# Kernel optimization log

Hardware: AMD Instinct MI355X
Metric: run time of the kernel (lower is better)

## Reference

```python
import jax, jax.numpy as jnp
import numpy as np

N, E, IN, OUT, R, B = 20000, 640000, 128, 128, 65, 65
BN_EPS = 1e-5


def setup_inputs() -> dict:
    key = jax.random.key(0)
    ks = jax.random.split(key, 8)
    node_feats = jax.random.normal(ks[0], (N, IN), dtype=jnp.float32)
    src = jax.random.randint(ks[1], (E,), 0, N, dtype=jnp.int32)
    dst = jax.random.randint(ks[2], (E,), 0, N, dtype=jnp.int32)
    etype = jax.random.randint(ks[3], (E,), 0, R, dtype=jnp.int32)
    norm = jax.random.uniform(ks[4], (E, 1), dtype=jnp.float32)
    basis = jax.random.normal(ks[5], (B, IN, OUT), dtype=jnp.float32) * 0.05
    comp = jax.random.normal(ks[6], (R, B), dtype=jnp.float32) * 0.1
    h_bias = jnp.zeros((OUT,), dtype=jnp.float32)
    W_res = jax.random.normal(ks[7], (IN, OUT), dtype=jnp.float32) * 0.05
    b_res = jnp.zeros((OUT,), dtype=jnp.float32)
    gamma = jnp.ones((OUT,), dtype=jnp.float32)
    beta = jnp.zeros((OUT,), dtype=jnp.float32)
    return dict(node_feats=node_feats, src=src, dst=dst, etype=etype, norm=norm,
                basis=basis, comp=comp, h_bias=h_bias, W_res=W_res, b_res=b_res,
                gamma=gamma, beta=beta)


def reference(node_feats, src, dst, etype, norm, basis, comp, h_bias, W_res, b_res, gamma, beta):
    n, in_f = node_feats.shape
    r = comp.shape[0]
    # Basis decomposition: W_r = sum_b comp[r,b] * basis[b]  -> (R, in, out)
    W = jnp.einsum('rb,bio->rio', comp, basis)
    # Per-edge message x[src] * norm (norm is scalar per edge so it commutes
    # with the relation matmul). Aggregate per (dst, relation) first, then do
    # one dense relation-batched GEMM (mathematically identical to DGL's
    # per-edge transform + scatter-add, since everything is linear).
    msg = node_feats[src] * norm                       # (E, in)
    seg = dst.astype(jnp.int32) * r + etype            # combined (dst, rel) key
    S = jax.ops.segment_sum(msg, seg, num_segments=n * r).reshape(n, r, in_f)
    h = jnp.einsum('nri,rio->no', S, W) + h_bias       # (N, out)
    h = jax.nn.relu(h)                                 # conv activation (dropout p=0)
    # Residual branch: relu(Linear(x))
    h = h + jax.nn.relu(node_feats @ W_res + b_res)
    # BatchNorm1d (training mode: batch stats, biased variance)
    mean = jnp.mean(h, axis=0)
    var = jnp.var(h, axis=0)
    h = (h - mean) * jax.lax.rsqrt(var + BN_EPS) * gamma + beta
    return h
```

## Files before the change

### kernel.cpp

```cpp
#include <hip/hip_runtime.h>
#include <hip/hip_bf16.h>


#define N_NODES 20000
#define E_EDGES 640000
#define R_REL   65
#define TM      64
#define NB_RESID 313
#define MAX_TILES 10240
#define SCAT_CH 2560

typedef __attribute__((ext_vector_type(8))) short bf16x8;
typedef __attribute__((ext_vector_type(4))) float f32x4;
typedef __attribute__((ext_vector_type(4))) unsigned int u32x4;
typedef __attribute__((ext_vector_type(2))) unsigned int u32x2;

__device__ __forceinline__ unsigned short f2bf(float x) {
    union { float f; unsigned int u; } c; c.f = x;
    unsigned int b = c.u + 0x7fffu + ((c.u >> 16) & 1u);
    return (unsigned short)(b >> 16);
}
__device__ __forceinline__ float bf2f_lo(unsigned int u) {
    union { unsigned int u; float f; } c; c.u = u << 16; return c.f;
}
__device__ __forceinline__ float bf2f_hi(unsigned int u) {
    union { unsigned int u; float f; } c; c.u = u & 0xffff0000u; return c.f;
}
__device__ __forceinline__ void async16(const void* g, void* l) {
    __builtin_amdgcn_global_load_lds(
        (const __attribute__((address_space(1))) unsigned int*)g,
        (__attribute__((address_space(3))) unsigned int*)l, 16, 0, 0);
}
__device__ __forceinline__ int unperm(int p) {
    return (p & 64) + ((p & 3) << 4) + ((p >> 2) & 15);
}

__global__ void k_prep1(const float* __restrict__ comp, const float* __restrict__ basis,
                        float* __restrict__ W32, const int* __restrict__ et,
                        const int* __restrict__ dstA, int* __restrict__ ghist,
                        int* __restrict__ gh2, const float* __restrict__ node_feats,
                        unsigned short* __restrict__ node_bf) {
    __shared__ float lc[16 * 65];
    __shared__ int lh[R_REL];
    int b = blockIdx.x, t = threadIdx.x;
    if (b < 320) {
        int r0 = (b >> 6) * 16;
        int col = (b & 63) * 256 + t;
        for (int j = t; j < 16 * 65; j += 256) {
            int rr = r0 + j / 65;
            lc[j] = (rr < R_REL) ? comp[rr * 65 + (j % 65)] : 0.f;
        }
        __syncthreads();
        float acc[16];
#pragma unroll
        for (int j = 0; j < 16; ++j) acc[j] = 0.f;
        for (int k = 0; k < 65; ++k) {
            float v = basis[k * 16384 + col];
#pragma unroll
            for (int j = 0; j < 16; ++j) acc[j] += lc[j * 65 + k] * v;
        }
#pragma unroll
        for (int j = 0; j < 16; ++j) {
            int rr = r0 + j;
            if (rr < R_REL) W32[rr * 16384 + col] = acc[j];
        }
    } else if (b < 832) {
        if (t < R_REL) lh[t] = 0;
        __syncthreads();
        for (int i = (b - 320) * 256 + t; i < E_EDGES; i += 512 * 256) {
            atomicAdd(&lh[et[i]], 1);
            atomicAdd(&gh2[dstA[i]], 1);
        }
        __syncthreads();
        if (t < R_REL) atomicAdd(&ghist[t], lh[t]);
    } else {
        int i = (b - 832) * 256 + t;
        if (i < N_NODES * 32) {
            float4 v = reinterpret_cast<const float4*>(node_feats)[i];
            __hip_bfloat162 b0 = __float22bfloat162_rn(make_float2(v.x, v.y));
            __hip_bfloat162 b1 = __float22bfloat162_rn(make_float2(v.z, v.w));
            u32x2 pk;
            pk.x = *reinterpret_cast<unsigned int*>(&b0);
            pk.y = *reinterpret_cast<unsigned int*>(&b1);
            reinterpret_cast<u32x2*>(node_bf)[i] = pk;
        }
    }
}

__global__ void k_prep2(const float* __restrict__ W32, unsigned short* __restrict__ Wt,
                        const float* __restrict__ Wresf, unsigned short* __restrict__ Wrest,
                        const int* __restrict__ gh2, int* __restrict__ bsum) {
    int b = blockIdx.x, t = threadIdx.x;
    if (b < 264) {
        __shared__ float tile[64][65];
        const float* s; unsigned short* d; int sub;
        if (b < R_REL * 4) { s = W32 + (size_t)(b >> 2) * 16384; d = Wt + (size_t)(b >> 2) * 16384; sub = b & 3; }
        else { s = Wresf; d = Wrest; sub = b - R_REL * 4; }
        int ot = (sub >> 1) & 1, itl = sub & 1;
        int tx = t & 63, ty = t >> 6;
        for (int it = 0; it < 16; ++it) {
            int i = ty + it * 4;
            tile[i][tx] = s[(itl * 64 + i) * 128 + ot * 64 + tx];
        }
        __syncthreads();
        for (int it = 0; it < 16; ++it) {
            int o = ty + it * 4;
            d[(ot * 64 + o) * 128 + itl * 64 + tx] = f2bf(tile[tx][o]);
        }
    } else {
        __shared__ int red[256];
        int i = (b - 264) * 256 + t;
        red[t] = (i < N_NODES) ? gh2[i] : 0;
        __syncthreads();
        for (int off = 128; off > 0; off >>= 1) {
            if (t < off) red[t] += red[t + off];
            __syncthreads();
        }
        if (t == 0) bsum[b - 264] = red[0];
    }
}

__global__ void k_prep3(const int* __restrict__ gh2, const int* __restrict__ bsum,
                        int* __restrict__ cnt2, int* __restrict__ seg,
                        const int* __restrict__ ghist, int* __restrict__ cnt,
                        int* __restrict__ ntiles_p, int* __restrict__ tile_rel,
                        int* __restrict__ tile_start, int* __restrict__ tile_len) {
    int b = blockIdx.x, t = threadIdx.x;
    if (b < 80) {
        __shared__ int red[256], spref;
        if (t < 64) {
            int v = (t < b) ? bsum[t] : 0;
            if (t < 16 && 64 + t < b) v += bsum[64 + t];
#pragma unroll
            for (int off = 1; off < 64; off <<= 1) v += __shfl_xor(v, off);
            if (t == 0) spref = v;
        }
        int i = b * 256 + t;
        int v = (i < N_NODES) ? gh2[i] : 0;
        red[t] = v;
        __syncthreads();
        for (int off = 1; off < 256; off <<= 1) {
            int x = (t >= off) ? red[t - off] : 0;
            __syncthreads();
            red[t] += x;
            __syncthreads();
        }
        int excl = red[t] - v + spref;
        if (i < N_NODES) {
            cnt2[i] = excl;
            seg[i] = excl;
            if (i == N_NODES - 1) seg[N_NODES] = excl + v;
        }
    } else {
        __shared__ int base[R_REL + 1], tbase[R_REL + 1];
        int lane = t & 63;
        if (t < 64) {
            int v = (lane < 64) ? ghist[lane] : 0;
            int x = v;
#pragma unroll
            for (int off = 1; off < 64; off <<= 1) {
                int y = __shfl_up(x, off);
                if (lane >= off) x += y;
            }
            base[lane] = x - v;
            if (lane == 63) {
                base[64] = x;
                base[65] = x + ghist[64];
            }
        }
        __syncthreads();
        if (t == 0) {
            int tb = 0;
            for (int r = 0; r < R_REL; ++r) {
                tbase[r] = tb;
                tb += (base[r + 1] - base[r] + TM - 1) / TM;
            }
            *ntiles_p = tb;
        }
        __syncthreads();
        if (t < R_REL) {
            cnt[t] = base[t];
            int s = base[t], e = base[t + 1], j = tbase[t];
            while (s < e) {
                int len = min(TM, e - s);
                tile_rel[j] = t; tile_start[j] = s; tile_len[j] = len;
                ++j; s += len;
            }
        }
    }
}

__global__ void k_scatter2(const int* __restrict__ et, const int* __restrict__ srcA,
                           const int* __restrict__ dstA, const float* __restrict__ norm,
                           int* __restrict__ cnt, int* __restrict__ cnt2,
                           int* __restrict__ srcp, float* __restrict__ normp,
                           int* __restrict__ inv2) {
    __shared__ int lh[R_REL], lbase[R_REL];
    int c0 = blockIdx.x * SCAT_CH;
    int cend = min(c0 + SCAT_CH, E_EDGES);
    if (threadIdx.x < R_REL) lh[threadIdx.x] = 0;
    __syncthreads();
    for (int i = c0 + threadIdx.x; i < cend; i += 256) atomicAdd(&lh[et[i]], 1);
    __syncthreads();
    if (threadIdx.x < R_REL && lh[threadIdx.x] > 0)
        lbase[threadIdx.x] = atomicAdd(&cnt[threadIdx.x], lh[threadIdx.x]);
    __syncthreads();
    if (threadIdx.x < R_REL) lh[threadIdx.x] = 0;
    __syncthreads();
    for (int i = c0 + threadIdx.x; i < cend; i += 256) {
        int r = et[i];
        int p = lbase[r] + atomicAdd(&lh[r], 1);
        srcp[p] = srcA[i];
        normp[p] = norm[i];
        inv2[p] = atomicAdd(&cnt2[dstA[i]], 1);
    }
}

__global__ __launch_bounds__(256, 3) void k_conv_gemm(
    const int* __restrict__ tile_rel, const int* __restrict__ tile_start,
    const int* __restrict__ tile_len, const int* __restrict__ ntiles_p,
    const int* __restrict__ srcp, const float* __restrict__ normp,
    const unsigned short* __restrict__ node_bf,
    const unsigned short* __restrict__ Wt, const unsigned short* __restrict__ Wrest,
    const float* __restrict__ b_res, const int* __restrict__ inv2,
    unsigned short* __restrict__ t_out, float* __restrict__ resid) {
    __shared__ unsigned short Alds[64 * 128];
    __shared__ unsigned short Blds[128 * 128];
    __shared__ float snorm[64];
    __shared__ int sp2[64];
    int t = threadIdx.x;
    int w = t >> 6, lane = t & 63;
    int wr = (w >> 1) * 32, wc = (w & 1) * 64;
    int lrow = lane & 15, quad = lane >> 4;

    if (blockIdx.x < NB_RESID) {
        int row0 = blockIdx.x * 64;
        int nrows = min(64, N_NODES - row0);
#pragma unroll
        for (int it = 0; it < 8; ++it) {
            int j = t + 256 * it;
            int o = j >> 4, c = j & 15, cs = c ^ (o & 15);
            async16(Wrest + o * 128 + cs * 8, &Blds[o * 128 + c * 8]);
        }
#pragma unroll
        for (int it = 0; it < 4; ++it) {
            int j = t + 256 * it;
            int p = j >> 4, c = j & 15, cs = c ^ (p & 15);
            if (p < nrows)
                async16(node_bf + (size_t)(row0 + p) * 128 + cs * 8,
                        &Alds[p * 128 + c * 8]);
        }
        __syncthreads();
        f32x4 acc[2][4];
#pragma unroll
        for (int i = 0; i < 2; ++i)
#pragma unroll
            for (int j = 0; j < 4; ++j) acc[i][j] = (f32x4){0.f, 0.f, 0.f, 0.f};
#pragma unroll
        for (int ks = 0; ks < 4; ++ks) {
            int cs = (ks * 4 + quad) ^ lrow;
            bf16x8 af[2], bfr[4];
#pragma unroll
            for (int i = 0; i < 2; ++i)
                af[i] = *reinterpret_cast<const bf16x8*>(&Alds[(wr + i * 16 + lrow) * 128 + cs * 8]);
#pragma unroll
            for (int j = 0; j < 4; ++j)
                bfr[j] = *reinterpret_cast<const bf16x8*>(&Blds[(wc + j * 16 + lrow) * 128 + cs * 8]);
#pragma unroll
            for (int i = 0; i < 2; ++i)
#pragma unroll
                for (int j = 0; j < 4; ++j)
                    acc[i][j] = __builtin_amdgcn_mfma_f32_16x16x32_bf16(af[i], bfr[j], acc[i][j], 0, 0, 0);
        }
        float br0 = b_res[wc + lrow];
        float br1 = b_res[wc + 16 + lrow];
        float br2 = b_res[wc + 32 + lrow];
        float br3 = b_res[wc + 48 + lrow];
#pragma unroll
        for (int i = 0; i < 2; ++i) {
#pragma unroll
            for (int reg = 0; reg < 4; ++reg) {
                int grow = row0 + wr + i * 16 + quad * 4 + reg;
                if (grow < N_NODES) {
                    float4 v;
                    v.x = fmaxf(acc[i][0][reg] + br0, 0.f);
                    v.y = fmaxf(acc[i][1][reg] + br1, 0.f);
                    v.z = fmaxf(acc[i][2][reg] + br2, 0.f);
                    v.w = fmaxf(acc[i][3][reg] + br3, 0.f);
                    *reinterpret_cast<float4*>(resid + (size_t)grow * 128 + wc + lrow * 4) = v;
                }
            }
        }
        return;
    }

    int tid = blockIdx.x - NB_RESID;
    if (tid >= *ntiles_p) return;
    int r = tile_rel[tid], start = tile_start[tid], len = tile_len[tid];
    const unsigned short* Wr = Wt + (size_t)r * 16384;
#pragma unroll
    for (int it = 0; it < 8; ++it) {
        int j = t + 256 * it;
        int o = j >> 4, c = j & 15, cs = c ^ (o & 15);
        async16(Wr + o * 128 + cs * 8, &Blds[o * 128 + c * 8]);
    }
#pragma unroll
    for (int it = 0; it < 4; ++it) {
        int j = t + 256 * it;
        int p = j >> 4, c = j & 15, cs = c ^ (p & 15);
        if (p < len)
            async16(node_bf + (size_t)srcp[start + p] * 128 + cs * 8,
                    &Alds[p * 128 + c * 8]);
    }
    if (t < TM && t < len) {
        snorm[t] = normp[start + t];
        sp2[t] = inv2[start + t];
    }
    __syncthreads();

    f32x4 acc[2][4];
#pragma unroll
    for (int i = 0; i < 2; ++i)
#pragma unroll
        for (int j = 0; j < 4; ++j) acc[i][j] = (f32x4){0.f, 0.f, 0.f, 0.f};
#pragma unroll
    for (int ks = 0; ks < 4; ++ks) {
        int cs = (ks * 4 + quad) ^ lrow;
        bf16x8 af[2], bfr[4];
#pragma unroll
        for (int i = 0; i < 2; ++i)
            af[i] = *reinterpret_cast<const bf16x8*>(&Alds[(wr + i * 16 + lrow) * 128 + cs * 8]);
#pragma unroll
        for (int j = 0; j < 4; ++j)
            bfr[j] = *reinterpret_cast<const bf16x8*>(&Blds[(wc + j * 16 + lrow) * 128 + cs * 8]);
#pragma unroll
        for (int i = 0; i < 2; ++i)
#pragma unroll
            for (int j = 0; j < 4; ++j)
                acc[i][j] = __builtin_amdgcn_mfma_f32_16x16x32_bf16(af[i], bfr[j], acc[i][j], 0, 0, 0);
    }

#pragma unroll
    for (int i = 0; i < 2; ++i) {
        int m0 = wr + i * 16 + quad * 4;
#pragma unroll
        for (int reg = 0; reg < 4; ++reg) {
            int m = m0 + reg;
            if (m < len) {
                float nm = snorm[m];
                int p2 = sp2[m];
                float2 lo2 = make_float2(acc[i][0][reg] * nm, acc[i][1][reg] * nm);
                float2 hi2 = make_float2(acc[i][2][reg] * nm, acc[i][3][reg] * nm);
                __hip_bfloat162 blo = __float22bfloat162_rn(lo2);
                __hip_bfloat162 bhi = __float22bfloat162_rn(hi2);
                u32x2 st;
                st.x = *reinterpret_cast<unsigned int*>(&blo);
                st.y = *reinterpret_cast<unsigned int*>(&bhi);
                __builtin_nontemporal_store(st,
                    reinterpret_cast<u32x2*>(t_out + (size_t)p2 * 128 + wc + lrow * 4));
            }
        }
    }
}

__global__ __launch_bounds__(256) void k_reduce_fused(
    const unsigned short* __restrict__ t, const int* __restrict__ seg,
    const float* __restrict__ resid, const float* __restrict__ h_bias,
    float* __restrict__ h, float* __restrict__ colsum, float* __restrict__ colsumsq) {
    __shared__ float cs1[128], cs2[128], sbias[128];
    if (threadIdx.x < 128) {
        cs1[threadIdx.x] = 0.f; cs2[threadIdx.x] = 0.f;
        sbias[threadIdx.x] = h_bias[unperm(threadIdx.x)];
    }
    __syncthreads();
    int w = threadIdx.x >> 6, lane = threadIdx.x & 63;
    int g = lane >> 4, c = lane & 15;
    for (int k = 0; k < 4; ++k) {
        int d = blockIdx.x * 16 + k * 4 + w;
        int a = seg[d], b = seg[d + 1];
        float s[8];
#pragma unroll
        for (int kk = 0; kk < 8; ++kk) s[kk] = 0.f;
        int q = a + g;
        for (; q + 12 < b; q += 16) {
            u32x4 v0 = __builtin_nontemporal_load(reinterpret_cast<const u32x4*>(t + (size_t)q * 128 + c * 8));
            u32x4 v1 = __builtin_nontemporal_load(reinterpret_cast<const u32x4*>(t + (size_t)(q + 4) * 128 + c * 8));
            u32x4 v2 = __builtin_nontemporal_load(reinterpret_cast<const u32x4*>(t + (size_t)(q + 8) * 128 + c * 8));
            u32x4 v3 = __builtin_nontemporal_load(reinterpret_cast<const u32x4*>(t + (size_t)(q + 12) * 128 + c * 8));
#pragma unroll
            for (int kk = 0; kk < 4; ++kk) {
                s[2 * kk]     += bf2f_lo(v0[kk]) + bf2f_lo(v1[kk]) + bf2f_lo(v2[kk]) + bf2f_lo(v3[kk]);
                s[2 * kk + 1] += bf2f_hi(v0[kk]) + bf2f_hi(v1[kk]) + bf2f_hi(v2[kk]) + bf2f_hi(v3[kk]);
            }
        }
        for (; q < b; q += 4) {
            u32x4 v = __builtin_nontemporal_load(reinterpret_cast<const u32x4*>(t + (size_t)q * 128 + c * 8));
#pragma unroll
            for (int kk = 0; kk < 4; ++kk) {
                s[2 * kk]     += bf2f_lo(v[kk]);
                s[2 * kk + 1] += bf2f_hi(v[kk]);
            }
        }
#pragma unroll
        for (int kk = 0; kk < 8; ++kk) {
            s[kk] += __shfl_xor(s[kk], 16);
            s[kk] += __shfl_xor(s[kk], 32);
        }
        if (g == 0) {
            const float* rp = resid + (size_t)d * 128 + c * 8;
            float4 r0 = *reinterpret_cast<const float4*>(rp);
            float4 r1 = *reinterpret_cast<const float4*>(rp + 4);
            float rr[8] = {r0.x, r0.y, r0.z, r0.w, r1.x, r1.y, r1.z, r1.w};
            float v[8];
#pragma unroll
            for (int kk = 0; kk < 8; ++kk)
                v[kk] = fmaxf(s[kk] + sbias[c * 8 + kk], 0.f) + rr[kk];
            float* hp = h + (size_t)d * 128 + c * 8;
            *reinterpret_cast<float4*>(hp)     = make_float4(v[0], v[1], v[2], v[3]);
            *reinterpret_cast<float4*>(hp + 4) = make_float4(v[4], v[5], v[6], v[7]);
#pragma unroll
            for (int kk = 0; kk < 8; ++kk) {
                atomicAdd(&cs1[c * 8 + kk], v[kk]);
                atomicAdd(&cs2[c * 8 + kk], v[kk] * v[kk]);
            }
        }
    }
    __syncthreads();
    if (threadIdx.x < 128) {
        atomicAdd(&colsum[threadIdx.x], cs1[threadIdx.x]);
        atomicAdd(&colsumsq[threadIdx.x], cs2[threadIdx.x]);
    }
}

__global__ void k_bn(float* __restrict__ h, const float* __restrict__ colsum,
                     const float* __restrict__ colsumsq, const float* __restrict__ gamma,
                     const float* __restrict__ beta) {
    __shared__ float sc[128], sh[128], tile[8][128];
    int t = threadIdx.x;
    if (t < 128) {
        int n = unperm(t);
        float m = colsum[t] * (1.f / N_NODES);
        float var = colsumsq[t] * (1.f / N_NODES) - m * m;
        float s = gamma[n] * rsqrtf(var + 1e-5f);
        sc[t] = s;
        sh[t] = beta[n] - m * s;
    }
    __syncthreads();
    int r = t >> 5;
    int p0 = (t & 31) * 4;
    int n0 = (p0 & 64) + ((p0 >> 2) & 15);
    for (int row0 = blockIdx.x * 8; row0 < N_NODES; row0 += gridDim.x * 8) {
        int row = row0 + r;
        float4 v = make_float4(0.f, 0.f, 0.f, 0.f);
        if (row < N_NODES) v = *reinterpret_cast<float4*>(h + (size_t)row * 128 + p0);
        v.x = v.x * sc[p0] + sh[p0];
        v.y = v.y * sc[p0 + 1] + sh[p0 + 1];
        v.z = v.z * sc[p0 + 2] + sh[p0 + 2];
        v.w = v.w * sc[p0 + 3] + sh[p0 + 3];
        tile[r][n0]      = v.x;
        tile[r][n0 + 16] = v.y;
        tile[r][n0 + 32] = v.z;
        tile[r][n0 + 48] = v.w;
        __syncthreads();
        if (row < N_NODES)
            *reinterpret_cast<float4*>(h + (size_t)row * 128 + p0) =
                *reinterpret_cast<float4*>(&tile[r][p0]);
        __syncthreads();
    }
}

extern "C" void kernel_launch(void* const* d_in, const int* in_sizes, int n_in,
                              void* d_out, int out_size, void* d_ws, size_t ws_size,
                              hipStream_t stream) {
    (void)in_sizes; (void)n_in; (void)out_size; (void)ws_size;
    const float* node_feats = (const float*)d_in[0];
    const int* src    = (const int*)d_in[1];
    const int* dst    = (const int*)d_in[2];
    const int* etype  = (const int*)d_in[3];
    const float* norm = (const float*)d_in[4];
    const float* basis = (const float*)d_in[5];
    const float* comp  = (const float*)d_in[6];
    const float* h_bias = (const float*)d_in[7];
    const float* W_res  = (const float*)d_in[8];
    const float* b_res  = (const float*)d_in[9];
    const float* gamma  = (const float*)d_in[10];
    const float* beta   = (const float*)d_in[11];

    char* ws = (char*)d_ws;
    int* ghist      = (int*)(ws + 0);
    int* cnt        = (int*)(ws + 1024);
    int* ntiles_p   = (int*)(ws + 2048);
    float* colsum   = (float*)(ws + 2560);
    float* colsumsq = (float*)(ws + 3072);
    int* bsum       = (int*)(ws + 3584);
    int* gh2        = (int*)(ws + 8192);
    int* tile_rel   = (int*)(ws + 88192);
    int* tile_start = (int*)(ws + 129152);
    int* tile_len   = (int*)(ws + 170112);
    unsigned short* Wt      = (unsigned short*)(ws + 211072);
    unsigned short* Wrest   = (unsigned short*)(ws + 2340992);
    unsigned short* node_bf = (unsigned short*)(ws + 2373760);
    int* srcp       = (int*)(ws + 7493760);
    float* normp    = (float*)(ws + 10053760);
    int* inv2       = (int*)(ws + 12613760);
    float* resid    = (float*)(ws + 15173760);
    int* seg        = (int*)(ws + 25413760);
    int* cnt2       = (int*)(ws + 25493776);
    const long T_BASE = 25573776L;
    float* W32      = (float*)(ws + T_BASE);
    unsigned short* t_buf = (unsigned short*)(ws + T_BASE);
    float* hacc = (float*)d_out;

    hipMemsetAsync(ws, 0, 88192, stream);
    k_prep1<<<3332, 256, 0, stream>>>(comp, basis, W32, etype, dst, ghist, gh2,
                                      node_feats, node_bf);
    k_prep2<<<344, 256, 0, stream>>>(W32, Wt, W_res, Wrest, gh2, bsum);
    k_prep3<<<81, 256, 0, stream>>>(gh2, bsum, cnt2, seg, ghist, cnt, ntiles_p,
                                    tile_rel, tile_start, tile_len);
    k_scatter2<<<(E_EDGES + SCAT_CH - 1) / SCAT_CH, 256, 0, stream>>>(
        etype, src, dst, norm, cnt, cnt2, srcp, normp, inv2);
    k_conv_gemm<<<NB_RESID + MAX_TILES, 256, 0, stream>>>(
        tile_rel, tile_start, tile_len, ntiles_p, srcp, normp, node_bf,
        Wt, Wrest, b_res, inv2, t_buf, resid);
    k_reduce_fused<<<N_NODES / 16, 256, 0, stream>>>(t_buf, seg, resid, h_bias,
                                                     hacc, colsum, colsumsq);
    k_bn<<<2500, 256, 0, stream>>>(hacc, colsum, colsumsq, gamma, beta);
}
```

Before: 352.9 us.

## Split conv GEMM tiles into column halves, merge prep kernels, deepen reduce unroll

The conv GEMM now gives each block half of the 128 output columns, which halves the B tile in LDS and the accumulator registers and raises launch bounds to 4 waves per SIMD. The grid doubles, so A gathers and edge metadata are loaded twice per tile. The two prep kernels merge into one, with each scan block recomputing its prefix directly from gh2 instead of using a separate block-sum pass. The reduce loop is unrolled to 8 loads in flight per iteration.

Result: slower. 387.8 us (+9.9%).

```diff
diff --git a/kernel.cpp b/kernel.cpp
--- a/kernel.cpp
+++ b/kernel.cpp
@@ -6,8 +6,8 @@
 #define E_EDGES 640000
 #define R_REL   65
 #define TM      64
-#define NB_RESID 313
-#define MAX_TILES 10240
+#define NB_RESID 626
+#define NB_EDGE  20608
 #define SCAT_CH 2560
 
 typedef __attribute__((ext_vector_type(8))) short bf16x8;
@@ -87,54 +87,27 @@
     }
 }
 
-__global__ void k_prep2(const float* __restrict__ W32, unsigned short* __restrict__ Wt,
-                        const float* __restrict__ Wresf, unsigned short* __restrict__ Wrest,
-                        const int* __restrict__ gh2, int* __restrict__ bsum) {
+__global__ void k_prep3(const int* __restrict__ gh2, int* __restrict__ cnt2,
+                        int* __restrict__ seg, const int* __restrict__ ghist,
+                        int* __restrict__ cnt, int* __restrict__ ntiles_p,
+                        int* __restrict__ tile_rel, int* __restrict__ tile_start,
+                        int* __restrict__ tile_len, const float* __restrict__ W32,
+                        unsigned short* __restrict__ Wt, const float* __restrict__ Wresf,
+                        unsigned short* __restrict__ Wrest) {
     int b = blockIdx.x, t = threadIdx.x;
-    if (b < 264) {
-        __shared__ float tile[64][65];
-        const float* s; unsigned short* d; int sub;
-        if (b < R_REL * 4) { s = W32 + (size_t)(b >> 2) * 16384; d = Wt + (size_t)(b >> 2) * 16384; sub = b & 3; }
-        else { s = Wresf; d = Wrest; sub = b - R_REL * 4; }
-        int ot = (sub >> 1) & 1, itl = sub & 1;
-        int tx = t & 63, ty = t >> 6;
-        for (int it = 0; it < 16; ++it) {
-            int i = ty + it * 4;
-            tile[i][tx] = s[(itl * 64 + i) * 128 + ot * 64 + tx];
-        }
-        __syncthreads();
-        for (int it = 0; it < 16; ++it) {
-            int o = ty + it * 4;
-            d[(ot * 64 + o) * 128 + itl * 64 + tx] = f2bf(tile[tx][o]);
-        }
-    } else {
+    if (b < 80) {
         __shared__ int red[256];
-        int i = (b - 264) * 256 + t;
-        red[t] = (i < N_NODES) ? gh2[i] : 0;
+        __shared__ int pref;
+        int acc = 0;
+        for (int i = t; i < b * 256; i += 256) acc += gh2[i];
+        red[t] = acc;
         __syncthreads();
         for (int off = 128; off > 0; off >>= 1) {
             if (t < off) red[t] += red[t + off];
             __syncthreads();
         }
-        if (t == 0) bsum[b - 264] = red[0];
-    }
-}
-
-__global__ void k_prep3(const int* __restrict__ gh2, const int* __restrict__ bsum,
-                        int* __restrict__ cnt2, int* __restrict__ seg,
-                        const int* __restrict__ ghist, int* __restrict__ cnt,
-                        int* __restrict__ ntiles_p, int* __restrict__ tile_rel,
-                        int* __restrict__ tile_start, int* __restrict__ tile_len) {
-    int b = blockIdx.x, t = threadIdx.x;
-    if (b < 80) {
-        __shared__ int red[256], spref;
-        if (t < 64) {
-            int v = (t < b) ? bsum[t] : 0;
-            if (t < 16 && 64 + t < b) v += bsum[64 + t];
-#pragma unroll
-            for (int off = 1; off < 64; off <<= 1) v += __shfl_xor(v, off);
-            if (t == 0) spref = v;
-        }
+        if (t == 0) pref = red[0];
+        __syncthreads();
         int i = b * 256 + t;
         int v = (i < N_NODES) ? gh2[i] : 0;
         red[t] = v;
@@ -145,17 +118,17 @@
             red[t] += x;
             __syncthreads();
         }
-        int excl = red[t] - v + spref;
+        int excl = red[t] - v + pref;
         if (i < N_NODES) {
             cnt2[i] = excl;
             seg[i] = excl;
             if (i == N_NODES - 1) seg[N_NODES] = excl + v;
         }
-    } else {
+    } else if (b == 80) {
         __shared__ int base[R_REL + 1], tbase[R_REL + 1];
         int lane = t & 63;
         if (t < 64) {
-            int v = (lane < 64) ? ghist[lane] : 0;
+            int v = ghist[lane];
             int x = v;
 #pragma unroll
             for (int off = 1; off < 64; off <<= 1) {
@@ -186,6 +159,23 @@
                 tile_rel[j] = t; tile_start[j] = s; tile_len[j] = len;
                 ++j; s += len;
             }
+        }
+    } else {
+        __shared__ float tile[64][65];
+        int bb = b - 81;
+        const float* s; unsigned short* d; int sub;
+        if (bb < R_REL * 4) { s = W32 + (size_t)(bb >> 2) * 16384; d = Wt + (size_t)(bb >> 2) * 16384; sub = bb & 3; }
+        else { s = Wresf; d = Wrest; sub = bb - R_REL * 4; }
+        int ot = (sub >> 1) & 1, itl = sub & 1;
+        int tx = t & 63, ty = t >> 6;
+        for (int it = 0; it < 16; ++it) {
+            int i = ty + it * 4;
+            tile[i][tx] = s[(itl * 64 + i) * 128 + ot * 64 + tx];
+        }
+        __syncthreads();
+        for (int it = 0; it < 16; ++it) {
+            int o = ty + it * 4;
+            d[(ot * 64 + o) * 128 + itl * 64 + tx] = f2bf(tile[tx][o]);
         }
     }
 }
@@ -216,7 +206,7 @@
     }
 }
 
-__global__ __launch_bounds__(256, 3) void k_conv_gemm(
+__global__ __launch_bounds__(256, 4) void k_conv_gemm(
     const int* __restrict__ tile_rel, const int* __restrict__ tile_start,
     const int* __restrict__ tile_len, const int* __restrict__ ntiles_p,
     const int* __restrict__ srcp, const float* __restrict__ normp,
@@ -225,22 +215,22 @@
     const float* __restrict__ b_res, const int* __restrict__ inv2,
     unsigned short* __restrict__ t_out, float* __restrict__ resid) {
     __shared__ unsigned short Alds[64 * 128];
-    __shared__ unsigned short Blds[128 * 128];
+    __shared__ unsigned short Blds[64 * 128];
     __shared__ float snorm[64];
     __shared__ int sp2[64];
     int t = threadIdx.x;
     int w = t >> 6, lane = t & 63;
-    int wr = (w >> 1) * 32, wc = (w & 1) * 64;
     int lrow = lane & 15, quad = lane >> 4;
 
     if (blockIdx.x < NB_RESID) {
-        int row0 = blockIdx.x * 64;
+        int rt = blockIdx.x >> 1, half = blockIdx.x & 1;
+        int row0 = rt * 64, wc = half * 64;
         int nrows = min(64, N_NODES - row0);
 #pragma unroll
-        for (int it = 0; it < 8; ++it) {
+        for (int it = 0; it < 4; ++it) {
             int j = t + 256 * it;
             int o = j >> 4, c = j & 15, cs = c ^ (o & 15);
-            async16(Wrest + o * 128 + cs * 8, &Blds[o * 128 + c * 8]);
+            async16(Wrest + (size_t)(wc + o) * 128 + cs * 8, &Blds[o * 128 + c * 8]);
         }
 #pragma unroll
         for (int it = 0; it < 4; ++it) {
@@ -251,55 +241,46 @@
                         &Alds[p * 128 + c * 8]);
         }
         __syncthreads();
-        f32x4 acc[2][4];
-#pragma unroll
-        for (int i = 0; i < 2; ++i)
-#pragma unroll
-            for (int j = 0; j < 4; ++j) acc[i][j] = (f32x4){0.f, 0.f, 0.f, 0.f};
+        f32x4 acc[4];
+#pragma unroll
+        for (int j = 0; j < 4; ++j) acc[j] = (f32x4){0.f, 0.f, 0.f, 0.f};
 #pragma unroll
         for (int ks = 0; ks < 4; ++ks) {
             int cs = (ks * 4 + quad) ^ lrow;
-            bf16x8 af[2], bfr[4];
-#pragma unroll
-            for (int i = 0; i < 2; ++i)
-                af[i] = *reinterpret_cast<const bf16x8*>(&Alds[(wr + i * 16 + lrow) * 128 + cs * 8]);
-#pragma unroll
-            for (int j = 0; j < 4; ++j)
-                bfr[j] = *reinterpret_cast<const bf16x8*>(&Blds[(wc + j * 16 + lrow) * 128 + cs * 8]);
-#pragma unroll
-            for (int i = 0; i < 2; ++i)
-#pragma unroll
-                for (int j = 0; j < 4; ++j)
-                    acc[i][j] = __builtin_amdgcn_mfma_f32_16x16x32_bf16(af[i], bfr[j], acc[i][j], 0, 0, 0);
+            bf16x8 af = *reinterpret_cast<const bf16x8*>(&Alds[(w * 16 + lrow) * 128 + cs * 8]);
+#pragma unroll
+            for (int j = 0; j < 4; ++j) {
+                bf16x8 bf = *reinterpret_cast<const bf16x8*>(&Blds[(j * 16 + lrow) * 128 + cs * 8]);
+                acc[j] = __builtin_amdgcn_mfma_f32_16x16x32_bf16(af, bf, acc[j], 0, 0, 0);
+            }
         }
         float br0 = b_res[wc + lrow];
         float br1 = b_res[wc + 16 + lrow];
         float br2 = b_res[wc + 32 + lrow];
         float br3 = b_res[wc + 48 + lrow];
 #pragma unroll
-        for (int i = 0; i < 2; ++i) {
-#pragma unroll
-            for (int reg = 0; reg < 4; ++reg) {
-                int grow = row0 + wr + i * 16 + quad * 4 + reg;
-                if (grow < N_NODES) {
-                    float4 v;
-                    v.x = fmaxf(acc[i][0][reg] + br0, 0.f);
-                    v.y = fmaxf(acc[i][1][reg] + br1, 0.f);
-                    v.z = fmaxf(acc[i][2][reg] + br2, 0.f);
-                    v.w = fmaxf(acc[i][3][reg] + br3, 0.f);
-                    *reinterpret_cast<float4*>(resid + (size_t)grow * 128 + wc + lrow * 4) = v;
-                }
+        for (int reg = 0; reg < 4; ++reg) {
+            int grow = row0 + w * 16 + quad * 4 + reg;
+            if (grow < N_NODES) {
+                float4 v;
+                v.x = fmaxf(acc[0][reg] + br0, 0.f);
+                v.y = fmaxf(acc[1][reg] + br1, 0.f);
+                v.z = fmaxf(acc[2][reg] + br2, 0.f);
+                v.w = fmaxf(acc[3][reg] + br3, 0.f);
+                *reinterpret_cast<float4*>(resid + (size_t)grow * 128 + wc + lrow * 4) = v;
             }
         }
         return;
     }
 
-    int tid = blockIdx.x - NB_RESID;
+    int q = blockIdx.x - NB_RESID;
+    int tid = q >> 1, half = q & 1;
     if (tid >= *ntiles_p) return;
     int r = tile_rel[tid], start = tile_start[tid], len = tile_len[tid];
-    const unsigned short* Wr = Wt + (size_t)r * 16384;
-#pragma unroll
-    for (int it = 0; it < 8; ++it) {
+    int wc = half * 64;
+    const unsigned short* Wr = Wt + (size_t)r * 16384 + (size_t)wc * 128;
+#pragma unroll
+    for (int it = 0; it < 4; ++it) {
         int j = t + 256 * it;
         int o = j >> 4, c = j & 15, cs = c ^ (o & 15);
         async16(Wr + o * 128 + cs * 8, &Blds[o * 128 + c * 8]);
@@ -318,47 +299,35 @@
     }
     __syncthreads();
 
-    f32x4 acc[2][4];
-#pragma unroll
-    for (int i = 0; i < 2; ++i)
-#pragma unroll
-        for (int j = 0; j < 4; ++j) acc[i][j] = (f32x4){0.f, 0.f, 0.f, 0.f};
+    f32x4 acc[4];
+#pragma unroll
+    for (int j = 0; j < 4; ++j) acc[j] = (f32x4){0.f, 0.f, 0.f, 0.f};
 #pragma unroll
     for (int ks = 0; ks < 4; ++ks) {
         int cs = (ks * 4 + quad) ^ lrow;
-        bf16x8 af[2], bfr[4];
-#pragma unroll
-        for (int i = 0; i < 2; ++i)
-            af[i] = *reinterpret_cast<const bf16x8*>(&Alds[(wr + i * 16 + lrow) * 128 + cs * 8]);
-#pragma unroll
-        for (int j = 0; j < 4; ++j)
-            bfr[j] = *reinterpret_cast<const bf16x8*>(&Blds[(wc + j * 16 + lrow) * 128 + cs * 8]);
-#pragma unroll
-        for (int i = 0; i < 2; ++i)
-#pragma unroll
-            for (int j = 0; j < 4; ++j)
-                acc[i][j] = __builtin_amdgcn_mfma_f32_16x16x32_bf16(af[i], bfr[j], acc[i][j], 0, 0, 0);
-    }
-
-#pragma unroll
-    for (int i = 0; i < 2; ++i) {
-        int m0 = wr + i * 16 + quad * 4;
-#pragma unroll
-        for (int reg = 0; reg < 4; ++reg) {
-            int m = m0 + reg;
-            if (m < len) {
-                float nm = snorm[m];
-                int p2 = sp2[m];
-                float2 lo2 = make_float2(acc[i][0][reg] * nm, acc[i][1][reg] * nm);
-                float2 hi2 = make_float2(acc[i][2][reg] * nm, acc[i][3][reg] * nm);
-                __hip_bfloat162 blo = __float22bfloat162_rn(lo2);
-                __hip_bfloat162 bhi = __float22bfloat162_rn(hi2);
-                u32x2 st;
-                st.x = *reinterpret_cast<unsigned int*>(&blo);
-                st.y = *reinterpret_cast<unsigned int*>(&bhi);
-                __builtin_nontemporal_store(st,
-                    reinterpret_cast<u32x2*>(t_out + (size_t)p2 * 128 + wc + lrow * 4));
-            }
+        bf16x8 af = *reinterpret_cast<const bf16x8*>(&Alds[(w * 16 + lrow) * 128 + cs * 8]);
+#pragma unroll
+        for (int j = 0; j < 4; ++j) {
+            bf16x8 bf = *reinterpret_cast<const bf16x8*>(&Blds[(j * 16 + lrow) * 128 + cs * 8]);
+            acc[j] = __builtin_amdgcn_mfma_f32_16x16x32_bf16(af, bf, acc[j], 0, 0, 0);
+        }
+    }
+
+#pragma unroll
+    for (int reg = 0; reg < 4; ++reg) {
+        int m = w * 16 + quad * 4 + reg;
+        if (m < len) {
+            float nm = snorm[m];
+            int p2 = sp2[m];
+            float2 lo2 = make_float2(acc[0][reg] * nm, acc[1][reg] * nm);
+            float2 hi2 = make_float2(acc[2][reg] * nm, acc[3][reg] * nm);
+            __hip_bfloat162 blo = __float22bfloat162_rn(lo2);
+            __hip_bfloat162 bhi = __float22bfloat162_rn(hi2);
+            u32x2 st;
+            st.x = *reinterpret_cast<unsigned int*>(&blo);
+            st.y = *reinterpret_cast<unsigned int*>(&bhi);
+            __builtin_nontemporal_store(st,
+                reinterpret_cast<u32x2*>(t_out + (size_t)p2 * 128 + wc + lrow * 4));
         }
     }
 }
@@ -382,15 +351,21 @@
 #pragma unroll
         for (int kk = 0; kk < 8; ++kk) s[kk] = 0.f;
         int q = a + g;
-        for (; q + 12 < b; q += 16) {
+        for (; q + 28 < b; q += 32) {
             u32x4 v0 = __builtin_nontemporal_load(reinterpret_cast<const u32x4*>(t + (size_t)q * 128 + c * 8));
             u32x4 v1 = __builtin_nontemporal_load(reinterpret_cast<const u32x4*>(t + (size_t)(q + 4) * 128 + c * 8));
             u32x4 v2 = __builtin_nontemporal_load(reinterpret_cast<const u32x4*>(t + (size_t)(q + 8) * 128 + c * 8));
             u32x4 v3 = __builtin_nontemporal_load(reinterpret_cast<const u32x4*>(t + (size_t)(q + 12) * 128 + c * 8));
+            u32x4 v4 = __builtin_nontemporal_load(reinterpret_cast<const u32x4*>(t + (size_t)(q + 16) * 128 + c * 8));
+            u32x4 v5 = __builtin_nontemporal_load(reinterpret_cast<const u32x4*>(t + (size_t)(q + 20) * 128 + c * 8));
+            u32x4 v6 = __builtin_nontemporal_load(reinterpret_cast<const u32x4*>(t + (size_t)(q + 24) * 128 + c * 8));
+            u32x4 v7 = __builtin_nontemporal_load(reinterpret_cast<const u32x4*>(t + (size_t)(q + 28) * 128 + c * 8));
 #pragma unroll
             for (int kk = 0; kk < 4; ++kk) {
-                s[2 * kk]     += bf2f_lo(v0[kk]) + bf2f_lo(v1[kk]) + bf2f_lo(v2[kk]) + bf2f_lo(v3[kk]);
-                s[2 * kk + 1] += bf2f_hi(v0[kk]) + bf2f_hi(v1[kk]) + bf2f_hi(v2[kk]) + bf2f_hi(v3[kk]);
+                s[2 * kk]     += bf2f_lo(v0[kk]) + bf2f_lo(v1[kk]) + bf2f_lo(v2[kk]) + bf2f_lo(v3[kk])
+                               + bf2f_lo(v4[kk]) + bf2f_lo(v5[kk]) + bf2f_lo(v6[kk]) + bf2f_lo(v7[kk]);
+                s[2 * kk + 1] += bf2f_hi(v0[kk]) + bf2f_hi(v1[kk]) + bf2f_hi(v2[kk]) + bf2f_hi(v3[kk])
+                               + bf2f_hi(v4[kk]) + bf2f_hi(v5[kk]) + bf2f_hi(v6[kk]) + bf2f_hi(v7[kk]);
             }
         }
         for (; q < b; q += 4) {
@@ -492,7 +467,6 @@
     int* ntiles_p   = (int*)(ws + 2048);
     float* colsum   = (float*)(ws + 2560);
     float* colsumsq = (float*)(ws + 3072);
-    int* bsum       = (int*)(ws + 3584);
     int* gh2        = (int*)(ws + 8192);
     int* tile_rel   = (int*)(ws + 88192);
     int* tile_start = (int*)(ws + 129152);
@@ -514,12 +488,12 @@
     hipMemsetAsync(ws, 0, 88192, stream);
     k_prep1<<<3332, 256, 0, stream>>>(comp, basis, W32, etype, dst, ghist, gh2,
                                       node_feats, node_bf);
-    k_prep2<<<344, 256, 0, stream>>>(W32, Wt, W_res, Wrest, gh2, bsum);
-    k_prep3<<<81, 256, 0, stream>>>(gh2, bsum, cnt2, seg, ghist, cnt, ntiles_p,
-                                    tile_rel, tile_start, tile_len);
+    k_prep3<<<345, 256, 0, stream>>>(gh2, cnt2, seg, ghist, cnt, ntiles_p,
+                                     tile_rel, tile_start, tile_len,
+                                     W32, Wt, W_res, Wrest);
     k_scatter2<<<(E_EDGES + SCAT_CH - 1) / SCAT_CH, 256, 0, stream>>>(
         etype, src, dst, norm, cnt, cnt2, srcp, normp, inv2);
-    k_conv_gemm<<<NB_RESID + MAX_TILES, 256, 0, stream>>>(
+    k_conv_gemm<<<NB_RESID + NB_EDGE, 256, 0, stream>>>(
         tile_rel, tile_start, tile_len, ntiles_p, srcp, normp, node_bf,
         Wt, Wrest, b_res, inv2, t_buf, resid);
     k_reduce_fused<<<N_NODES / 16, 256, 0, stream>>>(t_buf, seg, resid, h_bias,
```
